# Performance work log

Hardware: AMD Instinct MI355X
Metric: run time of the kernel (lower is better)

The kernel has to match this reference:

```python
import jax, jax.numpy as jnp
import numpy as np

# Static tree configuration: balanced binary tree branched to depth L; this layer splits level-L parents.
E = 32768   # n_events
F = 64      # n_features
G = 64      # global feature dim
B = 2       # n_branches
L = 3       # depth of current deepest level -> P = B**L parents to split
H = 256     # proj_nn hidden width
P = B ** L
D = L + 1   # degrees: parent itself (1) + L ancestors

def _off(l):
    # first node-row index of tree level l: E * (number of nodes in levels < l)
    return E * (B ** l - 1) // (B - 1)

def setup_inputs():
    key = jax.random.key(0)
    k0, k1, k2, k3 = jax.random.split(key, 4)
    N0 = _off(L + 1)  # 15 * E existing node rows
    x = jax.random.normal(k0, (N0, F), jnp.float32)
    global_features = jax.random.normal(k1, (E, G), jnp.float32)
    W1 = jax.random.normal(k2, (F + G, H), jnp.float32) / np.sqrt(F + G)
    b1 = jnp.zeros((H,), jnp.float32)
    W2 = jax.random.normal(k3, (H, B * F), jnp.float32) / np.sqrt(H)
    b2 = jnp.zeros((B * F,), jnp.float32)
    # event index of row off(l)+j*E+e is e for every node j (matches tile(arange(E)) layout)
    event = jnp.tile(jnp.arange(E, dtype=jnp.int32), N0 // E)
    # Rebuild existing edges exactly as prior applications of this layer would have:
    ar, arBE = np.arange(E), np.arange(B * E)
    edges, attrs = [], []
    for l in range(1, L + 1):              # level being created
        for p in range(B ** (l - 1)):       # parent index at level l-1
            children = _off(l) + p * B * E + arBE
            for d in range(1, l + 1):        # degree: 1 = parent, ... , l = root
                a = p // B ** (d - 1)         # ancestor node index at level l-d
                src = np.tile(_off(l - d) + a * E + ar, B)  # .repeat(B) on 1-D torch tensor tiles
                edges.append(np.vstack([src, children]))
                attrs.append(np.full(B * E, d))
    edge_index = jnp.asarray(np.hstack(edges), jnp.int32)
    edge_attr = jnp.asarray(np.concatenate(attrs), jnp.int32)
    return dict(x=x, edge_index=edge_index, edge_attr=edge_attr, event=event,
                global_features=global_features, W1=W1, b1=b1, W2=W2, b2=b2)

def reference(x, edge_index, edge_attr, event, global_features, W1, b1, W2, b2):
    N0 = x.shape[0]
    # --- per-parent gather + proj MLP, vectorized over the P parents of level L ---
    pidx = _off(L) + jnp.arange(P)[:, None] * E + jnp.arange(E)[None, :]      # (P, E)
    h = jnp.concatenate([x[pidx], global_features[event[pidx]]], axis=-1)    # (P, E, F+G)
    proj = jax.nn.relu(h @ W1 + b1) @ W2 + b2                                # (P, E, B*F)
    # reshape(-1, F): per parent rows ordered event-major, branch-minor; parents appended in order
    x_new = jnp.concatenate([x, proj.reshape(P * E * B, F)], axis=0)
    # --- new edges: per parent p, per degree d, source = ancestor idxs tiled B, target = children ---
    d = jnp.arange(1, D + 1)
    anc_off = jnp.asarray([_off(L - (dd - 1)) for dd in range(1, D + 1)])    # level of degree-d ancestor
    src_base = anc_off[None, :] + (jnp.arange(P)[:, None] // (B ** (d[None, :] - 1))) * E  # (P, D)
    src = src_base[:, :, None] + jnp.tile(jnp.arange(E), B)[None, None, :]   # (P, D, B*E)
    children = N0 + jnp.arange(P)[:, None] * (B * E) + jnp.arange(B * E)[None, :]  # (P, B*E)
    tgt = jnp.broadcast_to(children[:, None, :], (P, D, B * E))
    new_edges = jnp.stack([src.reshape(-1), tgt.reshape(-1)]).astype(edge_index.dtype)
    new_attr = jnp.broadcast_to(d[None, :, None], (P, D, B * E)).reshape(-1).astype(edge_attr.dtype)
    edge_index_new = jnp.concatenate([edge_index, new_edges], axis=1)
    edge_attr_new = jnp.concatenate([edge_attr, new_attr])
    event_new = jnp.concatenate([event, jnp.tile(jnp.arange(E, dtype=event.dtype), P * B)])
    return (x_new, edge_index_new, edge_attr_new, event_new)
```

## Files before the change

### kernel.cpp

```cpp
#include <hip/hip_runtime.h>

#define E      32768
#define F      64
#define G      64
#define B      2
#define L      3
#define H      256
#define P      8
#define D      4
#define N0     (15*E)
#define OFF3   (7*E)
#define NROWS  (P*E)
#define BE     (B*E)
#define EC0    1114112
#define ECN    (P*D*BE)
#define EC1    (EC0 + ECN)
#define NEV    (N0 + P*BE)

#define SXN   (NEV * F)
#define OXE   SXN
#define OEA   (OXE + 2*EC1)
#define OEV   (OEA + EC1)

using short8  = __attribute__((ext_vector_type(8))) short;
using floatx4 = __attribute__((ext_vector_type(4))) float;

__device__ __forceinline__ ushort f2b(float f) {
    unsigned u = __float_as_uint(f);
    return (ushort)((u + 0x7fffu + ((u >> 16) & 1u)) >> 16);
}

__global__ __launch_bounds__(256) void pack_kernel(const float* __restrict__ W1,
                                                   const float* __restrict__ W2,
                                                   ushort* __restrict__ wp) {
    int t = blockIdx.x * 256 + threadIdx.x;
    ushort tmp[8];
    if (t < 4096) {
        int lane = t & 63, nt = (t >> 6) & 3, kt = (t >> 8) & 3, w = (t >> 10) & 3;
        int col = w * 64 + nt * 16 + (lane & 15);
        int kb  = kt * 32 + (lane >> 4) * 8;
        #pragma unroll
        for (int j = 0; j < 8; ++j) tmp[j] = f2b(W1[(kb + j) * 256 + col]);
        uint4 v = make_uint4((unsigned)tmp[0] | ((unsigned)tmp[1] << 16),
                             (unsigned)tmp[2] | ((unsigned)tmp[3] << 16),
                             (unsigned)tmp[4] | ((unsigned)tmp[5] << 16),
                             (unsigned)tmp[6] | ((unsigned)tmp[7] << 16));
        *(uint4*)(wp + t * 8) = v;
    } else {
        int t2 = t - 4096;
        int lane = t2 & 63, nt = (t2 >> 6) & 1, kt = (t2 >> 7) & 7, w = (t2 >> 10) & 3;
        int col = w * 32 + nt * 16 + (lane & 15);
        int kb  = kt * 32 + (lane >> 4) * 8;
        #pragma unroll
        for (int j = 0; j < 8; ++j) tmp[j] = f2b(W2[(kb + j) * 128 + col]);
        uint4 v = make_uint4((unsigned)tmp[0] | ((unsigned)tmp[1] << 16),
                             (unsigned)tmp[2] | ((unsigned)tmp[3] << 16),
                             (unsigned)tmp[4] | ((unsigned)tmp[5] << 16),
                             (unsigned)tmp[6] | ((unsigned)tmp[7] << 16));
        *(uint4*)(wp + 32768 + t2 * 8) = v;
    }
}

__global__ __launch_bounds__(256) void copyx_kernel(const float4* __restrict__ x,
                                                    float4* __restrict__ out) {
    int i = blockIdx.x * 256 + threadIdx.x;
    if (i < (N0 * F) / 4) out[i] = x[i];
}

__global__ __launch_bounds__(256) void aux_kernel(const int* __restrict__ ei,
                                                  const int* __restrict__ ea,
                                                  const int* __restrict__ ev,
                                                  float* __restrict__ out) {
    int i4 = blockIdx.x * 256 + threadIdx.x;
    if (i4 < EC1 / 4) {
        int i = i4 * 4;
        float4 sf, tf, af;
        if (i < EC0) {
            int4 sv = ((const int4*)ei)[i4];
            int4 tv = ((const int4*)(ei + EC0))[i4];
            int4 av = ((const int4*)ea)[i4];
            sf = make_float4((float)sv.x, (float)sv.y, (float)sv.z, (float)sv.w);
            tf = make_float4((float)tv.x, (float)tv.y, (float)tv.z, (float)tv.w);
            af = make_float4((float)av.x, (float)av.y, (float)av.z, (float)av.w);
        } else {
            float s[4], t[4], a[4];
            #pragma unroll
            for (int q = 0; q < 4; ++q) {
                int k = i + q - EC0;
                int p = k >> 18;
                int r = k & (262144 - 1);
                int d = r >> 16;
                int j = r & (BE - 1);
                s[q] = (float)(E * (((8 >> d) - 1) + (p >> d)) + (j & (E - 1)));
                t[q] = (float)(N0 + p * BE + j);
                a[q] = (float)(d + 1);
            }
            sf = make_float4(s[0], s[1], s[2], s[3]);
            tf = make_float4(t[0], t[1], t[2], t[3]);
            af = make_float4(a[0], a[1], a[2], a[3]);
        }
        ((float4*)(out + OXE))[i4]       = sf;
        ((float4*)(out + OXE + EC1))[i4] = tf;
        ((float4*)(out + OEA))[i4]       = af;
    }
    if (i4 < NEV / 4) {
        int i = i4 * 4;
        float4 v;
        if (i < N0) {
            int4 e = ((const int4*)ev)[i4];
            v = make_float4((float)e.x, (float)e.y, (float)e.z, (float)e.w);
        } else {
            int base = (i - N0) & (E - 1);
            v = make_float4((float)base, (float)(base + 1), (float)(base + 2), (float)(base + 3));
        }
        ((float4*)(out + OEV))[i4] = v;
    }
}

#define HP1 136
#define HP2 264
__global__ __launch_bounds__(256, 2) void mlp_mfma(const float* __restrict__ x,
                                                   const float* __restrict__ gf,
                                                   const ushort* __restrict__ wpack,
                                                   const float* __restrict__ b1,
                                                   const float* __restrict__ b2,
                                                   float* __restrict__ out) {
    __shared__ ushort hsh[64 * HP1];
    __shared__ ushort hid[64 * HP2];
    const int tid  = threadIdx.x;
    const int wave = tid >> 6, lane = tid & 63;
    const int quad = lane >> 4, l16 = lane & 15;
    const int row0 = blockIdx.x * 64;

    short8 w1f[4][4];
    {
        const ushort* wp1 = wpack + wave * 8192;
        #pragma unroll
        for (int kt = 0; kt < 4; ++kt)
            #pragma unroll
            for (int nt = 0; nt < 4; ++nt)
                w1f[kt][nt] = *(const short8*)(wp1 + (kt * 4 + nt) * 512 + lane * 8);
    }
    short8 w2f[8][2];
    {
        const ushort* wp2 = wpack + 32768 + wave * 8192;
        #pragma unroll
        for (int kt = 0; kt < 8; ++kt)
            #pragma unroll
            for (int nt = 0; nt < 2; ++nt)
                w2f[kt][nt] = *(const short8*)(wp2 + (kt * 2 + nt) * 512 + lane * 8);
    }

    #pragma unroll
    for (int it = 0; it < 4; ++it) {
        int q  = tid + 256 * it;
        int r  = q >> 4;
        int cc = q & 15;
        int rg = row0 + r;
        const float* src = (cc < 8) ? (x + (OFF3 + rg) * 64 + cc * 8)
                                    : (gf + (rg & (E - 1)) * 64 + (cc - 8) * 8);
        float4 a  = *(const float4*)src;
        float4 bv = *(const float4*)(src + 4);
        uint4 v = make_uint4((unsigned)f2b(a.x)  | ((unsigned)f2b(a.y)  << 16),
                             (unsigned)f2b(a.z)  | ((unsigned)f2b(a.w)  << 16),
                             (unsigned)f2b(bv.x) | ((unsigned)f2b(bv.y) << 16),
                             (unsigned)f2b(bv.z) | ((unsigned)f2b(bv.w) << 16));
        *(uint4*)&hsh[r * HP1 + cc * 8] = v;
    }
    __syncthreads();

    {
        floatx4 acc[4][4];
        #pragma unroll
        for (int mt = 0; mt < 4; ++mt)
            #pragma unroll
            for (int nt = 0; nt < 4; ++nt)
                acc[mt][nt] = (floatx4){0.f, 0.f, 0.f, 0.f};
        #pragma unroll
        for (int mt = 0; mt < 4; ++mt) {
            short8 af[4];
            #pragma unroll
            for (int kt = 0; kt < 4; ++kt)
                af[kt] = *(const short8*)&hsh[(mt * 16 + l16) * HP1 + kt * 32 + quad * 8];
            #pragma unroll
            for (int nt = 0; nt < 4; ++nt)
                #pragma unroll
                for (int kt = 0; kt < 4; ++kt)
                    acc[mt][nt] = __builtin_amdgcn_mfma_f32_16x16x32_bf16(
                        af[kt], w1f[kt][nt], acc[mt][nt], 0, 0, 0);
        }
        #pragma unroll
        for (int nt = 0; nt < 4; ++nt) {
            int col = wave * 64 + nt * 16 + l16;
            float bb = b1[col];
            #pragma unroll
            for (int mt = 0; mt < 4; ++mt) {
                #pragma unroll
                for (int i = 0; i < 4; ++i) {
                    int m = mt * 16 + quad * 4 + i;
                    hid[m * HP2 + col] = f2b(fmaxf(acc[mt][nt][i] + bb, 0.f));
                }
            }
        }
    }
    __syncthreads();

    {
        floatx4 acc[4][2];
        #pragma unroll
        for (int mt = 0; mt < 4; ++mt)
            #pragma unroll
            for (int nt = 0; nt < 2; ++nt)
                acc[mt][nt] = (floatx4){0.f, 0.f, 0.f, 0.f};
        #pragma unroll
        for (int mt = 0; mt < 4; ++mt) {
            short8 hf[8];
            #pragma unroll
            for (int kt = 0; kt < 8; ++kt)
                hf[kt] = *(const short8*)&hid[(mt * 16 + l16) * HP2 + kt * 32 + quad * 8];
            #pragma unroll
            for (int nt = 0; nt < 2; ++nt)
                #pragma unroll
                for (int kt = 0; kt < 8; ++kt)
                    acc[mt][nt] = __builtin_amdgcn_mfma_f32_16x16x32_bf16(
                        hf[kt], w2f[kt][nt], acc[mt][nt], 0, 0, 0);
        }
        #pragma unroll
        for (int nt = 0; nt < 2; ++nt) {
            int col = wave * 32 + nt * 16 + l16;
            float bb = b2[col];
            #pragma unroll
            for (int mt = 0; mt < 4; ++mt) {
                #pragma unroll
                for (int i = 0; i < 4; ++i) {
                    int m = mt * 16 + quad * 4 + i;
                    out[N0 * F + (row0 + m) * 128 + col] = acc[mt][nt][i] + bb;
                }
            }
        }
    }
}

extern "C" void kernel_launch(void* const* d_in, const int* in_sizes, int n_in,
                              void* d_out, int out_size, void* d_ws, size_t ws_size,
                              hipStream_t stream) {
    const float* x  = (const float*)d_in[0];
    const int*   ei = (const int*)d_in[1];
    const int*   ea = (const int*)d_in[2];
    const int*   ev = (const int*)d_in[3];
    const float* gf = (const float*)d_in[4];
    const float* W1 = (const float*)d_in[5];
    const float* W2 = (const float*)d_in[7];
    const float* b1 = (const float*)d_in[6];
    const float* b2 = (const float*)d_in[8];
    float* out = (float*)d_out;
    ushort* wpack = (ushort*)d_ws;

    pack_kernel<<<32, 256, 0, stream>>>(W1, W2, wpack);
    mlp_mfma<<<NROWS / 64, 256, 0, stream>>>(x, gf, wpack, b1, b2, out);
    copyx_kernel<<<((N0 * F) / 4 + 255) / 256, 256, 0, stream>>>((const float4*)x,
                                                                 (float4*)out);
    aux_kernel<<<(EC1 / 4 + 255) / 256, 256, 0, stream>>>(ei, ea, ev, out);
}
```

Before: 464.8 us.

## Fuse MLP, x copy and edge/aux generation into one block-partitioned kernel

Merges the MLP, the bulk copy of x and the edge/event output kernel into a single launch whose blocks are split by index range, so the memory-bound copy and aux work can overlap with the MFMA blocks and launch gaps disappear. The MFMA operands are swapped so each lane holds four consecutive output columns, which allows vectorized bias loads and packed uint2/float4 stores for the hidden and output tiles. W2 fragments are now loaded after the first GEMM to shorten register live ranges. The copy and aux blocks now loop over several elements per thread. Risks are register pressure carried over from the MLP branch, which may limit occupancy for the simple blocks, and some load imbalance across block types.

```diff
diff --git a/kernel.cpp b/kernel.cpp
--- a/kernel.cpp
+++ b/kernel.cpp
@@ -22,6 +22,12 @@
 #define OEA   (OXE + 2*EC1)
 #define OEV   (OEA + EC1)
 
+#define MLP_BLOCKS   4096
+#define COPY_BLOCKS  3840
+#define AUX_BLOCKS   784
+#define AUX_STRIDE   (AUX_BLOCKS * 256)
+#define TOT_BLOCKS   (MLP_BLOCKS + COPY_BLOCKS + AUX_BLOCKS)
+
 using short8  = __attribute__((ext_vector_type(8))) short;
 using floatx4 = __attribute__((ext_vector_type(4))) float;
 
@@ -61,121 +67,61 @@
     }
 }
 
-__global__ __launch_bounds__(256) void copyx_kernel(const float4* __restrict__ x,
-                                                    float4* __restrict__ out) {
-    int i = blockIdx.x * 256 + threadIdx.x;
-    if (i < (N0 * F) / 4) out[i] = x[i];
-}
-
-__global__ __launch_bounds__(256) void aux_kernel(const int* __restrict__ ei,
-                                                  const int* __restrict__ ea,
-                                                  const int* __restrict__ ev,
-                                                  float* __restrict__ out) {
-    int i4 = blockIdx.x * 256 + threadIdx.x;
-    if (i4 < EC1 / 4) {
-        int i = i4 * 4;
-        float4 sf, tf, af;
-        if (i < EC0) {
-            int4 sv = ((const int4*)ei)[i4];
-            int4 tv = ((const int4*)(ei + EC0))[i4];
-            int4 av = ((const int4*)ea)[i4];
-            sf = make_float4((float)sv.x, (float)sv.y, (float)sv.z, (float)sv.w);
-            tf = make_float4((float)tv.x, (float)tv.y, (float)tv.z, (float)tv.w);
-            af = make_float4((float)av.x, (float)av.y, (float)av.z, (float)av.w);
-        } else {
-            float s[4], t[4], a[4];
-            #pragma unroll
-            for (int q = 0; q < 4; ++q) {
-                int k = i + q - EC0;
-                int p = k >> 18;
-                int r = k & (262144 - 1);
-                int d = r >> 16;
-                int j = r & (BE - 1);
-                s[q] = (float)(E * (((8 >> d) - 1) + (p >> d)) + (j & (E - 1)));
-                t[q] = (float)(N0 + p * BE + j);
-                a[q] = (float)(d + 1);
-            }
-            sf = make_float4(s[0], s[1], s[2], s[3]);
-            tf = make_float4(t[0], t[1], t[2], t[3]);
-            af = make_float4(a[0], a[1], a[2], a[3]);
-        }
-        ((float4*)(out + OXE))[i4]       = sf;
-        ((float4*)(out + OXE + EC1))[i4] = tf;
-        ((float4*)(out + OEA))[i4]       = af;
-    }
-    if (i4 < NEV / 4) {
-        int i = i4 * 4;
-        float4 v;
-        if (i < N0) {
-            int4 e = ((const int4*)ev)[i4];
-            v = make_float4((float)e.x, (float)e.y, (float)e.z, (float)e.w);
-        } else {
-            int base = (i - N0) & (E - 1);
-            v = make_float4((float)base, (float)(base + 1), (float)(base + 2), (float)(base + 3));
-        }
-        ((float4*)(out + OEV))[i4] = v;
-    }
-}
-
 #define HP1 136
 #define HP2 264
-__global__ __launch_bounds__(256, 2) void mlp_mfma(const float* __restrict__ x,
-                                                   const float* __restrict__ gf,
-                                                   const ushort* __restrict__ wpack,
-                                                   const float* __restrict__ b1,
-                                                   const float* __restrict__ b2,
-                                                   float* __restrict__ out) {
+__global__ __launch_bounds__(256, 2) void fused_kernel(const float* __restrict__ x,
+                                                       const float* __restrict__ gf,
+                                                       const ushort* __restrict__ wpack,
+                                                       const float* __restrict__ b1,
+                                                       const float* __restrict__ b2,
+                                                       const int* __restrict__ ei,
+                                                       const int* __restrict__ ea,
+                                                       const int* __restrict__ ev,
+                                                       float* __restrict__ out) {
     __shared__ ushort hsh[64 * HP1];
     __shared__ ushort hid[64 * HP2];
-    const int tid  = threadIdx.x;
-    const int wave = tid >> 6, lane = tid & 63;
-    const int quad = lane >> 4, l16 = lane & 15;
-    const int row0 = blockIdx.x * 64;
-
-    short8 w1f[4][4];
-    {
-        const ushort* wp1 = wpack + wave * 8192;
-        #pragma unroll
-        for (int kt = 0; kt < 4; ++kt)
+    const int bid = blockIdx.x;
+    const int tid = threadIdx.x;
+
+    if (bid < MLP_BLOCKS) {
+        const int wave = tid >> 6, lane = tid & 63;
+        const int quad = lane >> 4, l16 = lane & 15;
+        const int row0 = bid * 64;
+
+        short8 w1f[4][4];
+        {
+            const ushort* wp1 = wpack + wave * 8192;
+            #pragma unroll
+            for (int kt = 0; kt < 4; ++kt)
+                #pragma unroll
+                for (int nt = 0; nt < 4; ++nt)
+                    w1f[kt][nt] = *(const short8*)(wp1 + (kt * 4 + nt) * 512 + lane * 8);
+        }
+
+        #pragma unroll
+        for (int it = 0; it < 4; ++it) {
+            int q  = tid + 256 * it;
+            int r  = q >> 4;
+            int cc = q & 15;
+            int rg = row0 + r;
+            const float* src = (cc < 8) ? (x + (OFF3 + rg) * 64 + cc * 8)
+                                        : (gf + (rg & (E - 1)) * 64 + (cc - 8) * 8);
+            float4 a  = *(const float4*)src;
+            float4 bv = *(const float4*)(src + 4);
+            uint4 v = make_uint4((unsigned)f2b(a.x)  | ((unsigned)f2b(a.y)  << 16),
+                                 (unsigned)f2b(a.z)  | ((unsigned)f2b(a.w)  << 16),
+                                 (unsigned)f2b(bv.x) | ((unsigned)f2b(bv.y) << 16),
+                                 (unsigned)f2b(bv.z) | ((unsigned)f2b(bv.w) << 16));
+            *(uint4*)&hsh[r * HP1 + cc * 8] = v;
+        }
+        __syncthreads();
+
+        floatx4 acc1[4][4];
+        #pragma unroll
+        for (int mt = 0; mt < 4; ++mt)
             #pragma unroll
             for (int nt = 0; nt < 4; ++nt)
-                w1f[kt][nt] = *(const short8*)(wp1 + (kt * 4 + nt) * 512 + lane * 8);
-    }
-    short8 w2f[8][2];
-    {
-        const ushort* wp2 = wpack + 32768 + wave * 8192;
-        #pragma unroll
-        for (int kt = 0; kt < 8; ++kt)
-            #pragma unroll
-            for (int nt = 0; nt < 2; ++nt)
-                w2f[kt][nt] = *(const short8*)(wp2 + (kt * 2 + nt) * 512 + lane * 8);
-    }
-
-    #pragma unroll
-    for (int it = 0; it < 4; ++it) {
-        int q  = tid + 256 * it;
-        int r  = q >> 4;
-        int cc = q & 15;
-        int rg = row0 + r;
-        const float* src = (cc < 8) ? (x + (OFF3 + rg) * 64 + cc * 8)
-                                    : (gf + (rg & (E - 1)) * 64 + (cc - 8) * 8);
-        float4 a  = *(const float4*)src;
-        float4 bv = *(const float4*)(src + 4);
-        uint4 v = make_uint4((unsigned)f2b(a.x)  | ((unsigned)f2b(a.y)  << 16),
-                             (unsigned)f2b(a.z)  | ((unsigned)f2b(a.w)  << 16),
-                             (unsigned)f2b(bv.x) | ((unsigned)f2b(bv.y) << 16),
-                             (unsigned)f2b(bv.z) | ((unsigned)f2b(bv.w) << 16));
-        *(uint4*)&hsh[r * HP1 + cc * 8] = v;
-    }
-    __syncthreads();
-
-    {
-        floatx4 acc[4][4];
-        #pragma unroll
-        for (int mt = 0; mt < 4; ++mt)
-            #pragma unroll
-            for (int nt = 0; nt < 4; ++nt)
-                acc[mt][nt] = (floatx4){0.f, 0.f, 0.f, 0.f};
+                acc1[mt][nt] = (floatx4){0.f, 0.f, 0.f, 0.f};
         #pragma unroll
         for (int mt = 0; mt < 4; ++mt) {
             short8 af[4];
@@ -186,32 +132,42 @@
             for (int nt = 0; nt < 4; ++nt)
                 #pragma unroll
                 for (int kt = 0; kt < 4; ++kt)
-                    acc[mt][nt] = __builtin_amdgcn_mfma_f32_16x16x32_bf16(
-                        af[kt], w1f[kt][nt], acc[mt][nt], 0, 0, 0);
-        }
+                    acc1[mt][nt] = __builtin_amdgcn_mfma_f32_16x16x32_bf16(
+                        w1f[kt][nt], af[kt], acc1[mt][nt], 0, 0, 0);
+        }
+
+        short8 w2f[8][2];
+        {
+            const ushort* wp2 = wpack + 32768 + wave * 8192;
+            #pragma unroll
+            for (int kt = 0; kt < 8; ++kt)
+                #pragma unroll
+                for (int nt = 0; nt < 2; ++nt)
+                    w2f[kt][nt] = *(const short8*)(wp2 + (kt * 2 + nt) * 512 + lane * 8);
+        }
+
         #pragma unroll
         for (int nt = 0; nt < 4; ++nt) {
-            int col = wave * 64 + nt * 16 + l16;
-            float bb = b1[col];
+            float4 bb = *(const float4*)(b1 + wave * 64 + nt * 16 + quad * 4);
             #pragma unroll
             for (int mt = 0; mt < 4; ++mt) {
-                #pragma unroll
-                for (int i = 0; i < 4; ++i) {
-                    int m = mt * 16 + quad * 4 + i;
-                    hid[m * HP2 + col] = f2b(fmaxf(acc[mt][nt][i] + bb, 0.f));
-                }
-            }
-        }
-    }
-    __syncthreads();
-
-    {
-        floatx4 acc[4][2];
+                int m = mt * 16 + l16;
+                unsigned lo = (unsigned)f2b(fmaxf(acc1[mt][nt][0] + bb.x, 0.f)) |
+                              ((unsigned)f2b(fmaxf(acc1[mt][nt][1] + bb.y, 0.f)) << 16);
+                unsigned hi = (unsigned)f2b(fmaxf(acc1[mt][nt][2] + bb.z, 0.f)) |
+                              ((unsigned)f2b(fmaxf(acc1[mt][nt][3] + bb.w, 0.f)) << 16);
+                uint2 v = make_uint2(lo, hi);
+                *(uint2*)&hid[m * HP2 + wave * 64 + nt * 16 + quad * 4] = v;
+            }
+        }
+        __syncthreads();
+
+        floatx4 acc2[4][2];
         #pragma unroll
         for (int mt = 0; mt < 4; ++mt)
             #pragma unroll
             for (int nt = 0; nt < 2; ++nt)
-                acc[mt][nt] = (floatx4){0.f, 0.f, 0.f, 0.f};
+                acc2[mt][nt] = (floatx4){0.f, 0.f, 0.f, 0.f};
         #pragma unroll
         for (int mt = 0; mt < 4; ++mt) {
             short8 hf[8];
@@ -222,20 +178,77 @@
             for (int nt = 0; nt < 2; ++nt)
                 #pragma unroll
                 for (int kt = 0; kt < 8; ++kt)
-                    acc[mt][nt] = __builtin_amdgcn_mfma_f32_16x16x32_bf16(
-                        hf[kt], w2f[kt][nt], acc[mt][nt], 0, 0, 0);
+                    acc2[mt][nt] = __builtin_amdgcn_mfma_f32_16x16x32_bf16(
+                        w2f[kt][nt], hf[kt], acc2[mt][nt], 0, 0, 0);
         }
         #pragma unroll
         for (int nt = 0; nt < 2; ++nt) {
-            int col = wave * 32 + nt * 16 + l16;
-            float bb = b2[col];
+            float4 bb = *(const float4*)(b2 + wave * 32 + nt * 16 + quad * 4);
             #pragma unroll
             for (int mt = 0; mt < 4; ++mt) {
-                #pragma unroll
-                for (int i = 0; i < 4; ++i) {
-                    int m = mt * 16 + quad * 4 + i;
-                    out[N0 * F + (row0 + m) * 128 + col] = acc[mt][nt][i] + bb;
+                int m = mt * 16 + l16;
+                float4 v = make_float4(acc2[mt][nt][0] + bb.x, acc2[mt][nt][1] + bb.y,
+                                       acc2[mt][nt][2] + bb.z, acc2[mt][nt][3] + bb.w);
+                *(float4*)(out + N0 * F + (row0 + m) * 128 + wave * 32 + nt * 16 + quad * 4) = v;
+            }
+        }
+    } else if (bid < MLP_BLOCKS + COPY_BLOCKS) {
+        int cb = bid - MLP_BLOCKS;
+        const float4* src = (const float4*)x;
+        float4* dst = (float4*)out;
+        int base = cb * 2048 + tid;
+        float4 v[8];
+        #pragma unroll
+        for (int j = 0; j < 8; ++j) v[j] = src[base + j * 256];
+        #pragma unroll
+        for (int j = 0; j < 8; ++j) dst[base + j * 256] = v[j];
+    } else {
+        int ab = bid - MLP_BLOCKS - COPY_BLOCKS;
+        #pragma unroll
+        for (int it = 0; it < 4; ++it) {
+            int i4 = ab * 256 + tid + it * AUX_STRIDE;
+            if (i4 < EC1 / 4) {
+                int i = i4 * 4;
+                float4 sf, tf, af;
+                if (i < EC0) {
+                    int4 sv = ((const int4*)ei)[i4];
+                    int4 tv = ((const int4*)(ei + EC0))[i4];
+                    int4 av = ((const int4*)ea)[i4];
+                    sf = make_float4((float)sv.x, (float)sv.y, (float)sv.z, (float)sv.w);
+                    tf = make_float4((float)tv.x, (float)tv.y, (float)tv.z, (float)tv.w);
+                    af = make_float4((float)av.x, (float)av.y, (float)av.z, (float)av.w);
+                } else {
+                    float s[4], t[4], a[4];
+                    #pragma unroll
+                    for (int q = 0; q < 4; ++q) {
+                        int k = i + q - EC0;
+                        int p = k >> 18;
+                        int r = k & (262144 - 1);
+                        int d = r >> 16;
+                        int j = r & (BE - 1);
+                        s[q] = (float)(E * (((8 >> d) - 1) + (p >> d)) + (j & (E - 1)));
+                        t[q] = (float)(N0 + p * BE + j);
+                        a[q] = (float)(d + 1);
+                    }
+                    sf = make_float4(s[0], s[1], s[2], s[3]);
+                    tf = make_float4(t[0], t[1], t[2], t[3]);
+                    af = make_float4(a[0], a[1], a[2], a[3]);
                 }
+                ((float4*)(out + OXE))[i4]       = sf;
+                ((float4*)(out + OXE + EC1))[i4] = tf;
+                ((float4*)(out + OEA))[i4]       = af;
+            }
+            if (i4 < NEV / 4) {
+                int i = i4 * 4;
+                float4 v;
+                if (i < N0) {
+                    int4 e = ((const int4*)ev)[i4];
+                    v = make_float4((float)e.x, (float)e.y, (float)e.z, (float)e.w);
+                } else {
+                    int base = (i - N0) & (E - 1);
+                    v = make_float4((float)base, (float)(base + 1), (float)(base + 2), (float)(base + 3));
+                }
+                ((float4*)(out + OEV))[i4] = v;
             }
         }
     }
@@ -257,8 +270,6 @@
     ushort* wpack = (ushort*)d_ws;
 
     pack_kernel<<<32, 256, 0, stream>>>(W1, W2, wpack);
-    mlp_mfma<<<NROWS / 64, 256, 0, stream>>>(x, gf, wpack, b1, b2, out);
-    copyx_kernel<<<((N0 * F) / 4 + 255) / 256, 256, 0, stream>>>((const float4*)x,
-                                                                 (float4*)out);
-    aux_kernel<<<(EC1 / 4 + 255) / 256, 256, 0, stream>>>(ei, ea, ev, out);
-}
+    fused_kernel<<<TOT_BLOCKS, 256, 0, stream>>>(x, gf, wpack, b1, b2,
+                                                 ei, ea, ev, out);
+}
```

After: 461.8 us. No clear change (-0.7%).
